# Performance work log

Measured on AMD Instinct MI355X. Metric: run time of the kernel, lower is better.

## Reference

```python
import jax, jax.numpy as jnp
import numpy as np

T, H, NH, HD, I = 2048, 2048, 16, 128, 8192
EPS = 1e-6


def rotate_every_two(x):
    # result[..., 2i] = -x[..., 2i+1]; result[..., 2i+1] = x[..., 2i]
    x1 = x[..., ::2]
    x2 = x[..., 1::2]
    return jnp.stack((-x2, x1), axis=-1).reshape(x.shape)


def setup_inputs() -> dict:
    key = jax.random.key(0)
    ks = jax.random.split(key, 10)
    x = jax.random.normal(ks[0], (T, H), dtype=jnp.float32)
    normed_ages = jax.random.normal(ks[1], (T,), dtype=jnp.float32)
    sin = jax.random.uniform(ks[2], (T, 1, HD), dtype=jnp.float32)
    cos = jax.random.uniform(ks[3], (T, 1, HD), dtype=jnp.float32)
    attn_bias = jax.random.normal(ks[4], (1, NH, T, T), dtype=jnp.float32) * 0.02
    norm_w = jnp.ones((H,), dtype=jnp.float32)
    w_in = jax.random.normal(ks[5], (H, 3 * H + 2 * I), dtype=jnp.float32) / np.sqrt(H)
    b_in = jnp.zeros((3 * H + 2 * I,), dtype=jnp.float32)
    w_out = jax.random.normal(ks[6], (H + I, H), dtype=jnp.float32) / np.sqrt(H + I)
    b_out = jnp.zeros((H,), dtype=jnp.float32)
    return {"x": x, "normed_ages": normed_ages, "sin": sin, "cos": cos,
            "attn_bias": attn_bias, "norm_w": norm_w, "w_in": w_in,
            "b_in": b_in, "w_out": w_out, "b_out": b_out}


def reference(x, normed_ages, sin, cos, attn_bias, norm_w, b_in, b_out, w_in, w_out):
    # RMSNorm
    xn = x * jax.lax.rsqrt(jnp.mean(x * x, axis=-1, keepdims=True) + EPS) * norm_w
    # use_normed_ages: overwrite last two feature columns
    xn = xn.at[:, -2].set(normed_ages)
    xn = xn.at[:, -1].set(normed_ages * normed_ages)
    # fused input projection: [T, 2I (ff) | 3H (qkv)]
    t = xn @ w_in + b_in
    ff = t[:, : 2 * I]
    qkv = t[:, 2 * I:].reshape(T, 3, NH, HD)
    q = qkv[:, 0] * cos + rotate_every_two(qkv[:, 0]) * sin  # [T, NH, HD]
    k = qkv[:, 1] * cos + rotate_every_two(qkv[:, 1]) * sin
    v = qkv[:, 2]
    # attention (xformers memory_efficient_attention semantics, scale 1/sqrt(HD))
    scores = jnp.einsum('thd,shd->hts', q, k) / np.sqrt(HD) + attn_bias[0]
    probs = jax.nn.softmax(scores, axis=-1)
    attn = jnp.einsum('hts,shd->thd', probs, v).reshape(T, H)
    # SwiGLU
    x1, x2 = ff[:, :I], ff[:, I:]
    ff = jax.nn.silu(x1) * x2
    combined = jnp.concatenate((attn, ff), axis=-1)  # [T, H+I]
    return combined @ w_out + b_out
```

## Files before the change

kernel.cpp:

```cpp
#include <hip/hip_runtime.h>
#include <stdint.h>

typedef unsigned short u16;
typedef __attribute__((ext_vector_type(8))) short short8;
typedef __attribute__((ext_vector_type(4))) short short4v;
typedef __attribute__((ext_vector_type(4))) float floatx4;

#define T_DIM 2048
#define NH    16
#define HD    128
#define H_DIM 2048
#define I_DIM 8192
#define NCOL1 22528
#define NCOL2 10240
#define PADW  1036
#define KSPLIT 4
#define KSLEN  (NCOL2 / KSPLIT)

__device__ __forceinline__ float bf2f(u16 b) {
  union { uint32_t u; float f; } x; x.u = ((uint32_t)b) << 16; return x.f;
}
__device__ __forceinline__ u16 f2bf(float f) {
  union { float f; uint32_t u; } x; x.f = f;
  uint32_t r = x.u + 0x7fffu + ((x.u >> 16) & 1u);
  return (u16)(r >> 16);
}

__device__ __forceinline__ void gl_lds16(const void* g, void* l) {
  __builtin_amdgcn_global_load_lds((const __attribute__((address_space(1))) void*)g,
                                   (__attribute__((address_space(3))) void*)l, 16, 0, 0);
}

__device__ __forceinline__ floatx4 mfma32(short8 a, short8 b, floatx4 c) {
  return __builtin_amdgcn_mfma_f32_16x16x32_bf16(a, b, c, 0, 0, 0);
}
__device__ __forceinline__ floatx4 mfma16(short4v a, short4v b, floatx4 c) {
#if __has_builtin(__builtin_amdgcn_mfma_f32_16x16x16bf16_1k)
  return __builtin_amdgcn_mfma_f32_16x16x16bf16_1k(a, b, c, 0, 0, 0);
#else
  asm volatile("v_mfma_f32_16x16x16_bf16 %0, %1, %2, %0" : "+v"(c) : "v"(a), "v"(b));
  return c;
#endif
}

__global__ __launch_bounds__(256) void rmsnorm_k(
    const float* __restrict__ x, const float* __restrict__ ages,
    const float* __restrict__ w, u16* __restrict__ xn) {
  int t = blockIdx.x, tid = threadIdx.x;
  const float* xr = x + (size_t)t * H_DIM;
  floatx4 a = *(const floatx4*)(xr + tid * 8);
  floatx4 b = *(const floatx4*)(xr + tid * 8 + 4);
  float ss = a[0]*a[0]+a[1]*a[1]+a[2]*a[2]+a[3]*a[3]
           + b[0]*b[0]+b[1]*b[1]+b[2]*b[2]+b[3]*b[3];
#pragma unroll
  for (int off = 32; off >= 1; off >>= 1) ss += __shfl_xor(ss, off);
  __shared__ float red[4];
  if ((tid & 63) == 0) red[tid >> 6] = ss;
  __syncthreads();
  float tot = red[0] + red[1] + red[2] + red[3];
  float rms = rsqrtf(tot * (1.0f / H_DIM) + 1e-6f);
  const float* wr = w + tid * 8;
  float v[8] = {a[0],a[1],a[2],a[3],b[0],b[1],b[2],b[3]};
  short8 o;
#pragma unroll
  for (int i = 0; i < 8; ++i) o[i] = (short)f2bf(v[i] * rms * wr[i]);
  if (tid == 255) {
    float ag = ages[t];
    o[6] = (short)f2bf(ag);
    o[7] = (short)f2bf(ag * ag);
  }
  *(short8*)(xn + (size_t)t * H_DIM + tid * 8) = o;
}

__global__ __launch_bounds__(256) void transpose_f32_bf16(
    const float* __restrict__ in, u16* __restrict__ out, int K, int N) {
  __shared__ float tile[32][33];
  int n0 = blockIdx.x * 32, k0 = blockIdx.y * 32;
  int c = threadIdx.x & 31, r = threadIdx.x >> 5;
#pragma unroll
  for (int i = 0; i < 4; ++i) {
    int kk = r + i * 8;
    tile[c][kk] = in[(size_t)(k0 + kk) * N + n0 + c];
  }
  __syncthreads();
#pragma unroll
  for (int i = 0; i < 4; ++i) {
    int nn = r + i * 8;
    out[(size_t)(n0 + nn) * K + k0 + c] = f2bf(tile[nn][c]);
  }
}

template<int OUTF>
__global__ __launch_bounds__(256, 2) void gemm_bt(
    const u16* __restrict__ A, const u16* __restrict__ B,
    const float* __restrict__ bias, void* __restrict__ Cout,
    int M, int N, int K, int klen) {
  __shared__ u16 As[4096];
  __shared__ u16 Bs[4096];
  int nbm = M >> 7, nbn = N >> 7;
  int per = nbm * nbn;
  int nwg = per * (K / klen);
  int bid = blockIdx.x;
  int swz = (bid & 7) * (nwg >> 3) + (bid >> 3);
  int sp = swz / per, r = swz % per;
  int bn = r / nbm, bm = r % nbm;
  int kbeg = sp * klen;
  int tid = threadIdx.x, lane = tid & 63;
  int wr = tid >> 7, wc = (tid >> 6) & 1;
  int lq = lane & 15, lg = lane >> 4;

  int r0 = tid >> 2, kc0 = (tid & 3) << 3;
  const u16* Ag0 = A + (size_t)(bm * 128 + r0) * K + kc0;
  const u16* Ag1 = Ag0 + (size_t)64 * K;
  const u16* Bg0 = B + (size_t)(bn * 128 + r0) * K + kc0;
  const u16* Bg1 = Bg0 + (size_t)64 * K;
  u16* As0 = As + tid * 8;
  u16* As1 = As + 2048 + tid * 8;
  u16* Bs0 = Bs + tid * 8;
  u16* Bs1 = Bs + 2048 + tid * 8;

  const u16* Ard = As + (wr * 64 + lq) * 32 + lg * 8;
  const u16* Brd = Bs + (wc * 64 + lq) * 32 + lg * 8;

  floatx4 acc[4][4] = {};

  for (int kt = kbeg; kt < kbeg + klen; kt += 32) {
    __syncthreads();
    gl_lds16(Ag0 + kt, As0);
    gl_lds16(Ag1 + kt, As1);
    gl_lds16(Bg0 + kt, Bs0);
    gl_lds16(Bg1 + kt, Bs1);
    __syncthreads();
    short8 af[4], bfr[4];
#pragma unroll
    for (int i = 0; i < 4; ++i) af[i]  = *(const short8*)(Ard + i * 512);
#pragma unroll
    for (int i = 0; i < 4; ++i) bfr[i] = *(const short8*)(Brd + i * 512);
#pragma unroll
    for (int mi = 0; mi < 4; ++mi)
#pragma unroll
      for (int ni = 0; ni < 4; ++ni)
        acc[mi][ni] = mfma32(af[mi], bfr[ni], acc[mi][ni]);
  }

#pragma unroll
  for (int mi = 0; mi < 4; ++mi) {
#pragma unroll
    for (int ni = 0; ni < 4; ++ni) {
      int col = bn * 128 + wc * 64 + ni * 16 + lq;
      float bv = (OUTF == 2) ? 0.f : bias[col];
#pragma unroll
      for (int j = 0; j < 4; ++j) {
        int row = bm * 128 + wr * 64 + mi * 16 + lg * 4 + j;
        float vv = acc[mi][ni][j] + bv;
        if (OUTF == 0)      ((u16*)Cout)[(size_t)row * N + col] = f2bf(vv);
        else if (OUTF == 1) ((float*)Cout)[(size_t)row * N + col] = vv;
        else ((float*)Cout)[(size_t)sp * M * N + (size_t)row * N + col] = vv;
      }
    }
  }
}

__global__ __launch_bounds__(256) void reduce_split(
    const float* __restrict__ part, const float* __restrict__ bias,
    float* __restrict__ out) {
  size_t idx = ((size_t)blockIdx.x * 256 + threadIdx.x) * 4;
  int col = (int)(idx & (H_DIM - 1));
  floatx4 acc = *(const floatx4*)(bias + col);
#pragma unroll
  for (int s = 0; s < KSPLIT; ++s) {
    floatx4 p = *(const floatx4*)(part + (size_t)s * T_DIM * H_DIM + idx);
#pragma unroll
    for (int j = 0; j < 4; ++j) acc[j] += p[j];
  }
  *(floatx4*)(out + idx) = acc;
}

__global__ __launch_bounds__(256) void rope_split(
    const u16* __restrict__ tb, const float* __restrict__ sinp, const float* __restrict__ cosp,
    u16* __restrict__ qb, u16* __restrict__ kf, u16* __restrict__ vf) {
  __shared__ u16 vtile[32][130];
  int t0 = blockIdx.x * 32, h = blockIdx.y, tid = threadIdx.x;
  int r = tid >> 3, d0 = (tid & 7) << 4;
  int t = t0 + r;
  const u16* base = tb + (size_t)t * NCOL1 + 2 * I_DIM + h * HD + d0;
  const float* cp = cosp + (size_t)t * HD + d0;
  const float* sp = sinp + (size_t)t * HD + d0;
  float cv[16], sv[16];
#pragma unroll
  for (int i = 0; i < 16; i += 4) {
    *(floatx4*)(cv + i) = *(const floatx4*)(cp + i);
    *(floatx4*)(sv + i) = *(const floatx4*)(sp + i);
  }
#pragma unroll
  for (int s = 0; s < 2; ++s) {
    const u16* src = base + s * (NH * HD);
    short8 x0 = *(const short8*)src;
    short8 x1 = *(const short8*)(src + 8);
    float xf[16];
#pragma unroll
    for (int i = 0; i < 8; ++i) { xf[i] = bf2f((u16)x0[i]); xf[8 + i] = bf2f((u16)x1[i]); }
    short8 o0, o1;
#pragma unroll
    for (int i = 0; i < 8; i += 2) {
      o0[i]     = (short)f2bf(xf[i] * cv[i] - xf[i + 1] * sv[i]);
      o0[i + 1] = (short)f2bf(xf[i + 1] * cv[i + 1] + xf[i] * sv[i + 1]);
      o1[i]     = (short)f2bf(xf[8 + i] * cv[8 + i] - xf[9 + i] * sv[8 + i]);
      o1[i + 1] = (short)f2bf(xf[9 + i] * cv[9 + i] + xf[8 + i] * sv[9 + i]);
    }
    if (s == 0) {
      u16* dst = qb + ((size_t)h * T_DIM + t) * HD + d0;
      *(short8*)dst = o0;
      *(short8*)(dst + 8) = o1;
    } else {
      int s16 = t >> 4, tt = d0 >> 5, lg0 = (d0 >> 3) & 3;
      size_t cb = (((size_t)h * 128 + s16) * 4 + tt) * 512 + ((t & 15) + 16 * lg0) * 8;
      *(short8*)(kf + cb) = o0;
      *(short8*)(kf + cb + 128) = o1;
    }
  }
  short8 v0 = *(const short8*)(base + 2 * NH * HD);
  short8 v1 = *(const short8*)(base + 2 * NH * HD + 8);
#pragma unroll
  for (int i = 0; i < 8; ++i) {
    vtile[r][d0 + i]     = (u16)v0[i];
    vtile[r][d0 + 8 + i] = (u16)v1[i];
  }
  __syncthreads();
  {
    int d = tid >> 1, th = (tid & 1) << 4;
    int s16 = (t0 + th) >> 4;
    int dp = d >> 5, par = (d >> 4) & 1, lqv = d & 15;
    size_t cb = (((size_t)h * 128 + s16) * 4 + dp) * 512 + par * 4;
#pragma unroll
    for (int lg = 0; lg < 4; ++lg) {
      short4v g;
#pragma unroll
      for (int j = 0; j < 4; ++j) g[j] = (short)vtile[th + lg * 4 + j][d];
      *(short4v*)(vf + cb + (size_t)(lqv + 16 * lg) * 8) = g;
    }
  }
}

__global__ __launch_bounds__(256) void silu_mul(
    const u16* __restrict__ tb, u16* __restrict__ comb) {
  int idx = blockIdx.x * 256 + threadIdx.x;
  int t = idx >> 10;
  int j = (idx & 1023) << 3;
  const u16* p1 = tb + (size_t)t * NCOL1 + j;
  const u16* p2 = p1 + I_DIM;
  short8 a = *(const short8*)p1;
  short8 b = *(const short8*)p2;
  short8 o;
#pragma unroll
  for (int i = 0; i < 8; ++i) {
    float x1 = bf2f((u16)a[i]), x2 = bf2f((u16)b[i]);
    float s = x1 / (1.0f + __expf(-x1));
    o[i] = (short)f2bf(s * x2);
  }
  *(short8*)(comb + (size_t)t * NCOL2 + H_DIM + j) = o;
}

__global__ __launch_bounds__(256) void attn_fused(
    const u16* __restrict__ Q, const u16* __restrict__ kf,
    const u16* __restrict__ vf, const float* __restrict__ bias,
    u16* __restrict__ comb) {
  __shared__ float lds[16 * PADW];
  int bid = blockIdx.x;
  int swz = (bid & 7) * 256 + (bid >> 3);
  int h = swz >> 7, qt = swz & 127;
  int q0 = qt * 16;
  int tid = threadIdx.x;
  int w = tid >> 6, lane = tid & 63;
  int lq = lane & 15, lg = lane >> 4;

  const u16* Qp = Q + ((size_t)h * T_DIM + q0 + lq) * HD + lg * 8;
  const u16* Kf = kf + ((size_t)h * 128) * 2048 + lane * 8;
  const u16* Vf = vf + ((size_t)h * 128) * 2048 + lane * 8;
  const float* Bh = bias + ((size_t)h * T_DIM + q0) * T_DIM;

  short8 qf[4];
#pragma unroll
  for (int t = 0; t < 4; ++t) qf[t] = *(const short8*)(Qp + t * 32);

  floatx4 o[8] = {};
  float m = -1e30f, l = 0.f;
  const float sc = 0.08838834764831845f;

#pragma unroll
  for (int tile = 0; tile < 2; ++tile) {
#pragma unroll
    for (int r = 0; r < 16; ++r) {
      const float* src = Bh + (size_t)r * T_DIM + tile * 1024 + tid * 4;
      gl_lds16(src, &lds[r * PADW + tid * 4]);
    }
    __syncthreads();
#pragma unroll
    for (int sub = 0; sub < 8; ++sub) {
      int soff = sub * 128 + w * 32;
      int s0 = tile * 1024 + soff;
      int s16a = s0 >> 4;
      const u16* ka = Kf + (size_t)s16a * 2048;
      floatx4 st0 = {0.f,0.f,0.f,0.f}, st1 = {0.f,0.f,0.f,0.f};
#pragma unroll
      for (int t = 0; t < 4; ++t) {
        st0 = mfma32(*(const short8*)(ka + t * 512), qf[t], st0);
        st1 = mfma32(*(const short8*)(ka + 2048 + t * 512), qf[t], st1);
      }
      floatx4 b0 = *(const floatx4*)&lds[lq * PADW + soff + lg * 4];
      floatx4 b1 = *(const floatx4*)&lds[lq * PADW + soff + lg * 4 + 16];
      float p[8]; float tmax = -1e30f;
#pragma unroll
      for (int j = 0; j < 4; ++j) {
        p[j]     = st0[j] * sc + b0[j];
        p[4 + j] = st1[j] * sc + b1[j];
        tmax = fmaxf(tmax, fmaxf(p[j], p[4 + j]));
      }
      tmax = fmaxf(tmax, __shfl_xor(tmax, 16));
      tmax = fmaxf(tmax, __shfl_xor(tmax, 32));
      float mn = fmaxf(m, tmax);
      float alpha = __expf(m - mn);
      float rs = 0.f;
      short4v pb0, pb1;
#pragma unroll
      for (int j = 0; j < 4; ++j) {
        float e0 = __expf(p[j] - mn), e1 = __expf(p[4 + j] - mn);
        rs += e0 + e1;
        pb0[j] = (short)f2bf(e0);
        pb1[j] = (short)f2bf(e1);
      }
      rs += __shfl_xor(rs, 16);
      rs += __shfl_xor(rs, 32);
      l = l * alpha + rs; m = mn;
#pragma unroll
      for (int dt = 0; dt < 8; ++dt) o[dt] *= alpha;
      const u16* vb = Vf + (size_t)s16a * 2048;
#pragma unroll
      for (int dp = 0; dp < 4; ++dp) {
        short8 wa = *(const short8*)(vb + dp * 512);
        short8 wb = *(const short8*)(vb + 2048 + dp * 512);
        short4v a0 = {wa[0], wa[1], wa[2], wa[3]};
        short4v a1 = {wa[4], wa[5], wa[6], wa[7]};
        short4v c0 = {wb[0], wb[1], wb[2], wb[3]};
        short4v c1 = {wb[4], wb[5], wb[6], wb[7]};
        o[2*dp]     = mfma16(a0, pb0, o[2*dp]);
        o[2*dp + 1] = mfma16(a1, pb0, o[2*dp + 1]);
        o[2*dp]     = mfma16(c0, pb1, o[2*dp]);
        o[2*dp + 1] = mfma16(c1, pb1, o[2*dp + 1]);
      }
    }
    __syncthreads();
  }

  if (lg == 0) { lds[8448 + w * 16 + lq] = m; lds[8512 + w * 16 + lq] = l; }
  __syncthreads();
  float M = -1e30f;
#pragma unroll
  for (int i = 0; i < 4; ++i) M = fmaxf(M, lds[8448 + i * 16 + lq]);
  float scale = __expf(m - M);
#pragma unroll
  for (int dt = 0; dt < 8; ++dt) {
    floatx4 so = o[dt] * scale;
    *(floatx4*)&lds[w * 2112 + lq * 132 + dt * 16 + lg * 4] = so;
  }
  __syncthreads();
  {
    int row = tid >> 4, d0 = (tid & 15) * 8;
    float M2 = -1e30f;
#pragma unroll
    for (int i = 0; i < 4; ++i) M2 = fmaxf(M2, lds[8448 + i * 16 + row]);
    float den = 0.f;
#pragma unroll
    for (int i = 0; i < 4; ++i)
      den += __expf(lds[8448 + i * 16 + row] - M2) * lds[8512 + i * 16 + row];
    float inv = 1.0f / den;
    short8 ov;
#pragma unroll
    for (int k = 0; k < 8; ++k) {
      float s = 0.f;
#pragma unroll
      for (int i = 0; i < 4; ++i) s += lds[i * 2112 + row * 132 + d0 + k];
      ov[k] = (short)f2bf(s * inv);
    }
    *(short8*)(comb + (size_t)(q0 + row) * NCOL2 + h * HD + d0) = ov;
  }
}

extern "C" void kernel_launch(void* const* d_in, const int* in_sizes, int n_in,
                              void* d_out, int out_size, void* d_ws, size_t ws_size,
                              hipStream_t stream) {
  (void)in_sizes; (void)n_in; (void)out_size; (void)ws_size;
  const float* x     = (const float*)d_in[0];
  const float* ages  = (const float*)d_in[1];
  const float* sinp  = (const float*)d_in[2];
  const float* cosp  = (const float*)d_in[3];
  const float* bias  = (const float*)d_in[4];
  const float* normw = (const float*)d_in[5];
  const float* w_in  = (const float*)d_in[6];
  const float* b_in  = (const float*)d_in[7];
  const float* w_out = (const float*)d_in[8];
  const float* b_out = (const float*)d_in[9];

  char* ws = (char*)d_ws;
  const size_t SZ_XN   = (size_t)T_DIM * H_DIM * 2;
  const size_t SZ_W1T  = (size_t)NCOL1 * H_DIM * 2;
  const size_t SZ_T    = (size_t)T_DIM * NCOL1 * 2;
  const size_t SZ_HEAD = (size_t)NH * T_DIM * HD * 2;
  u16* xn   = (u16*)(ws);
  u16* w1t  = (u16*)(ws + SZ_XN);
  u16* tb   = (u16*)(ws + SZ_XN + SZ_W1T);
  u16* qb   = (u16*)(ws + SZ_XN + SZ_W1T + SZ_T);
  u16* kf   = (u16*)(ws + SZ_XN + SZ_W1T + SZ_T + SZ_HEAD);
  u16* vf   = (u16*)(ws + SZ_XN + SZ_W1T + SZ_T + 2 * SZ_HEAD);
  u16* w2t  = (u16*)(ws + SZ_XN);
  u16* comb = (u16*)(ws + SZ_XN + (48ull << 20));
  float* part = (float*)tb;

  rmsnorm_k<<<T_DIM, 256, 0, stream>>>(x, ages, normw, xn);
  transpose_f32_bf16<<<dim3(NCOL1 / 32, H_DIM / 32), 256, 0, stream>>>(w_in, w1t, H_DIM, NCOL1);
  gemm_bt<0><<<(T_DIM / 128) * (NCOL1 / 128), 256, 0, stream>>>(
      xn, w1t, b_in, tb, T_DIM, NCOL1, H_DIM, H_DIM);
  rope_split<<<dim3(T_DIM / 32, NH), 256, 0, stream>>>(tb, sinp, cosp, qb, kf, vf);
  silu_mul<<<(T_DIM * I_DIM) / (256 * 8), 256, 0, stream>>>(tb, comb);
  transpose_f32_bf16<<<dim3(H_DIM / 32, NCOL2 / 32), 256, 0, stream>>>(w_out, w2t, NCOL2, H_DIM);
  attn_fused<<<NH * (T_DIM / 16), 256, 0, stream>>>(qb, kf, vf, bias, comb);
  gemm_bt<2><<<(T_DIM / 128) * (H_DIM / 128) * KSPLIT, 256, 0, stream>>>(
      comb, w2t, b_out, part, T_DIM, H_DIM, NCOL2, KSLEN);
  reduce_split<<<(T_DIM * H_DIM / 4) / 256, 256, 0, stream>>>(part, b_out, (float*)d_out);
}
```

Baseline: 603.3 us.

## Pipeline GEMM main loop with 4-stage LDS ring and XOR-swizzled layout

Replaces the single-buffered global-to-LDS load plus two barriers per k-step with a 4-slot LDS ring that prefetches three tiles ahead. It synchronises with explicit vmcnt waits and one barrier per iteration. LDS rows are XOR-swizzled on both the store and read side to avoid bank conflicts, and MFMA issue is wrapped in s_setprio. LDS use grows to 64KB per block, which may limit occupancy below the two blocks per CU the launch bounds request.

```diff
diff --git a/kernel.cpp b/kernel.cpp
--- a/kernel.cpp
+++ b/kernel.cpp
@@ -95,52 +95,66 @@
     const u16* __restrict__ A, const u16* __restrict__ B,
     const float* __restrict__ bias, void* __restrict__ Cout,
     int M, int N, int K, int klen) {
-  __shared__ u16 As[4096];
-  __shared__ u16 Bs[4096];
+  __shared__ __align__(16) u16 sm[32768];
   int nbm = M >> 7, nbn = N >> 7;
   int per = nbm * nbn;
   int nwg = per * (K / klen);
   int bid = blockIdx.x;
   int swz = (bid & 7) * (nwg >> 3) + (bid >> 3);
-  int sp = swz / per, r = swz % per;
-  int bn = r / nbm, bm = r % nbm;
+  int sp = swz / per, rr = swz % per;
+  int bn = rr / nbm, bm = rr % nbm;
   int kbeg = sp * klen;
-  int tid = threadIdx.x, lane = tid & 63;
+  int tid = threadIdx.x, lane = tid & 63, w = tid >> 6;
   int wr = tid >> 7, wc = (tid >> 6) & 1;
   int lq = lane & 15, lg = lane >> 4;
 
-  int r0 = tid >> 2, kc0 = (tid & 3) << 3;
-  const u16* Ag0 = A + (size_t)(bm * 128 + r0) * K + kc0;
-  const u16* Ag1 = Ag0 + (size_t)64 * K;
-  const u16* Bg0 = B + (size_t)(bn * 128 + r0) * K + kc0;
-  const u16* Bg1 = Bg0 + (size_t)64 * K;
-  u16* As0 = As + tid * 8;
-  u16* As1 = As + 2048 + tid * 8;
-  u16* Bs0 = Bs + tid * 8;
-  u16* Bs1 = Bs + 2048 + tid * 8;
-
-  const u16* Ard = As + (wr * 64 + lq) * 32 + lg * 8;
-  const u16* Brd = Bs + (wc * 64 + lq) * 32 + lg * 8;
+  int srow = lane >> 2;
+  int scol = (((lane & 3) ^ ((lane >> 3) & 3)) << 3);
+  const u16* Ag0 = A + (size_t)(bm * 128 + w * 32 + srow) * K + kbeg + scol;
+  const u16* Ag1 = Ag0 + (size_t)16 * K;
+  const u16* Bg0 = B + (size_t)(bn * 128 + w * 32 + srow) * K + kbeg + scol;
+  const u16* Bg1 = Bg0 + (size_t)16 * K;
+  u16* Ad0 = sm + w * 1024 + lane * 8;
+  u16* Ad1 = Ad0 + 512;
+  u16* Bd0 = sm + 4096 + w * 1024 + lane * 8;
+  u16* Bd1 = Bd0 + 512;
+
+  int xorc = ((lq >> 1) & 3) << 3;
+  int aoff = (wr * 64 + lq) * 32 + ((lg * 8) ^ xorc);
+  int boff = 4096 + (wc * 64 + lq) * 32 + ((lg * 8) ^ xorc);
 
   floatx4 acc[4][4] = {};
-
-  for (int kt = kbeg; kt < kbeg + klen; kt += 32) {
-    __syncthreads();
-    gl_lds16(Ag0 + kt, As0);
-    gl_lds16(Ag1 + kt, As1);
-    gl_lds16(Bg0 + kt, Bs0);
-    gl_lds16(Bg1 + kt, Bs1);
-    __syncthreads();
-    short8 af[4], bfr[4];
-#pragma unroll
-    for (int i = 0; i < 4; ++i) af[i]  = *(const short8*)(Ard + i * 512);
-#pragma unroll
-    for (int i = 0; i < 4; ++i) bfr[i] = *(const short8*)(Brd + i * 512);
+  const int NT = klen >> 5;
+
+  auto STAGE = [&](int t) {
+    int sl = (t & 3) * 8192;
+    int ko = t * 32;
+    gl_lds16(Ag0 + ko, Ad0 + sl);
+    gl_lds16(Ag1 + ko, Ad1 + sl);
+    gl_lds16(Bg0 + ko, Bd0 + sl);
+    gl_lds16(Bg1 + ko, Bd1 + sl);
+  };
+
+  STAGE(0); STAGE(1); STAGE(2);
+  asm volatile("s_waitcnt vmcnt(8)\n\ts_barrier" ::: "memory");
+
+  for (int t = 0; t < NT; ++t) {
+    if (t + 3 < NT) STAGE(t + 3);
+    const u16* sb = sm + (t & 3) * 8192;
+    short8 af[4], bf[4];
+#pragma unroll
+    for (int i = 0; i < 4; ++i) af[i] = *(const short8*)(sb + aoff + i * 512);
+#pragma unroll
+    for (int i = 0; i < 4; ++i) bf[i] = *(const short8*)(sb + boff + i * 512);
+    __builtin_amdgcn_s_setprio(1);
 #pragma unroll
     for (int mi = 0; mi < 4; ++mi)
 #pragma unroll
       for (int ni = 0; ni < 4; ++ni)
-        acc[mi][ni] = mfma32(af[mi], bfr[ni], acc[mi][ni]);
+        acc[mi][ni] = mfma32(af[mi], bf[ni], acc[mi][ni]);
+    __builtin_amdgcn_s_setprio(0);
+    if (t + 3 < NT) asm volatile("s_waitcnt vmcnt(8)\n\ts_barrier" ::: "memory");
+    else            asm volatile("s_waitcnt vmcnt(0)\n\ts_barrier" ::: "memory");
   }
 
 #pragma unroll
```

After: 612.3 us. About the same (+1.5%).
